# Kernel optimization log

Measured on AMD Instinct MI355X. Metric: run time of the kernel, lower is better.

The kernel has to match this reference:

```python
import jax, jax.numpy as jnp
import numpy as np

EPS = 1e-5
GROUPS = 8

def group_norm(x, w, b):
    B, C, H, W = x.shape
    xg = x.reshape(B, GROUPS, C // GROUPS, H, W)
    mean = xg.mean(axis=(2, 3, 4), keepdims=True)
    var = xg.var(axis=(2, 3, 4), keepdims=True)
    xn = ((xg - mean) * jax.lax.rsqrt(var + EPS)).reshape(B, C, H, W)
    return xn * w[None, :, None, None] + b[None, :, None, None]

def conv1x1(x, w, b):
    # x: [B,C,H,W], w: [O,C] -> [B,O,H,W]
    return jnp.einsum('bchw,oc->bohw', x, w) + b[None, :, None, None]

def setup_inputs() -> dict:
    key = jax.random.key(0)
    ks = jax.random.split(key, 16)
    C, Ci = 256, 128
    B, H, W = 4, 64, 64
    s3 = 1.0 / np.sqrt(C * 9)
    s1 = 1.0 / np.sqrt(C)
    return {
        'x': jax.random.normal(ks[0], (B, C, H, W), jnp.float32),
        'smooth_w': jax.random.uniform(ks[1], (C, C, 3, 3), jnp.float32, -s3, s3),
        'smooth_b': jax.random.uniform(ks[2], (C,), jnp.float32, -s3, s3),
        'gn1_w': jnp.ones((C,), jnp.float32),
        'gn1_b': jnp.zeros((C,), jnp.float32),
        'g_w': jax.random.uniform(ks[3], (Ci, C), jnp.float32, -s1, s1),
        'g_b': jax.random.uniform(ks[4], (Ci,), jnp.float32, -s1, s1),
        'theta_w': jax.random.uniform(ks[5], (Ci, C), jnp.float32, -s1, s1),
        'theta_b': jax.random.uniform(ks[6], (Ci,), jnp.float32, -s1, s1),
        'phi_w': jax.random.uniform(ks[7], (Ci, C), jnp.float32, -s1, s1),
        'phi_b': jax.random.uniform(ks[8], (Ci,), jnp.float32, -s1, s1),
        'w_w': 0.01 * jax.random.normal(ks[9], (C, Ci), jnp.float32),
        'w_b': jnp.zeros((C,), jnp.float32),
        'gn2_w': jnp.ones((C,), jnp.float32),
        'gn2_b': jnp.zeros((C,), jnp.float32),
    }

def reference(x, smooth_w, smooth_b, gn1_w, gn1_b, g_w, g_b, theta_w, theta_b,
              phi_w, phi_b, w_w, w_b, gn2_w, gn2_b):
    # input_smooth: 3x3 conv + GroupNorm(8) + ReLU
    xs = jax.lax.conv_general_dilated(
        x, smooth_w, window_strides=(1, 1), padding='SAME',
        dimension_numbers=('NCHW', 'OIHW', 'NCHW')) + smooth_b[None, :, None, None]
    xs = jax.nn.relu(group_norm(xs, gn1_w, gn1_b))
    B, C, H, W = xs.shape
    Ci = g_w.shape[0]
    N = H * W
    g_x = conv1x1(xs, g_w, g_b).reshape(B, Ci, N).transpose(0, 2, 1)      # [B,N,Ci]
    theta_x = conv1x1(xs, theta_w, theta_b).reshape(B, Ci, N).transpose(0, 2, 1)  # [B,N,Ci]
    phi_x = conv1x1(xs, phi_w, phi_b).reshape(B, Ci, N)                   # [B,Ci,N]
    f = jnp.einsum('bnc,bcm->bnm', theta_x, phi_x)                        # [B,N,N]
    attn = jax.nn.softmax(f, axis=-1)
    y = jnp.einsum('bnm,bmc->bnc', attn, g_x)                             # [B,N,Ci]
    y = y.transpose(0, 2, 1).reshape(B, Ci, H, W)
    w_y = group_norm(conv1x1(y, w_w, w_b), gn2_w, gn2_b)
    return w_y * 0.1 + xs
```

## Files before the change

### kernel.cpp

```cpp
#include <hip/hip_runtime.h>
#include <math.h>

#define Bn 4
#define Cn 256
#define CIn 128
#define Hn 64
#define Wn 64
#define Nn 4096
#define Gn 8
#define CPGn 32
#define EPSc 1e-5f

typedef unsigned short ushort_t;
typedef short bfrag __attribute__((ext_vector_type(8)));
typedef float f32x4 __attribute__((ext_vector_type(4)));
typedef ushort_t u16x8 __attribute__((ext_vector_type(8)));

static __device__ __forceinline__ ushort_t f2bf(float f) {
  unsigned u = __float_as_uint(f);
  return (ushort_t)((u + 0x7FFFu + ((u >> 16) & 1u)) >> 16);
}

static __device__ __forceinline__ unsigned cvt_pk_bf16(float lo, float hi) {
  unsigned r;
  asm("v_cvt_pk_bf16_f32 %0, %1, %2" : "=v"(r) : "v"(lo), "v"(hi));
  return r;
}

static __device__ __forceinline__ float bf2f(ushort_t u) {
  return __uint_as_float((unsigned)u << 16);
}

static __device__ __forceinline__ void gl_lds16(const ushort_t* g, ushort_t* l) {
  __builtin_amdgcn_global_load_lds(
      (__attribute__((address_space(1))) void*)g,
      (__attribute__((address_space(3))) void*)l, 16, 0, 0);
}

__global__ __launch_bounds__(256) void k_prepack(
    const float* __restrict__ w3, const float* __restrict__ thw,
    const float* __restrict__ phw, const float* __restrict__ gww,
    const float* __restrict__ ww,
    ushort_t* __restrict__ w9, ushort_t* __restrict__ wp9,
    ushort_t* __restrict__ wwb) {
  int i = blockIdx.x * 256 + threadIdx.x;
  if (i < 589824) {
    float v = w3[i];
    int co = i / 2304, r = i % 2304, ci = r / 9, tap = r % 9;
    w9[tap * 65536 + co * 256 + ci] = f2bf(v);
  } else if (i < 688128) {
    int j = i - 589824;
    int which = j >> 15, r = j & 32767;
    const float* src = (which == 0) ? thw : (which == 1) ? phw : gww;
    wp9[j] = f2bf(src[r]);
  } else if (i < 720896) {
    int j = i - 688128;
    wwb[j] = f2bf(ww[j]);
  }
}

__global__ __launch_bounds__(512) void k_conv_mfma(
    const float* __restrict__ x, const ushort_t* __restrict__ w9,
    const float* __restrict__ b3, float* __restrict__ out,
    float* __restrict__ part) {
  __shared__ __align__(16) ushort_t lx[3 * 66 * 128];
  const int tid = threadIdx.x;
  const int lane = tid & 63, w = tid >> 6;
  const int ln = lane & 15, lhi = lane >> 4;
  const int h = blockIdx.x, b = blockIdx.y;
  const int wco = w * 32;

  f32x4 acc[2][4];
#pragma unroll
  for (int mf = 0; mf < 2; ++mf)
#pragma unroll
    for (int nf = 0; nf < 4; ++nf) acc[mf][nf] = (f32x4){0.f, 0.f, 0.f, 0.f};

  for (int cc = 0; cc < 2; ++cc) {
    __syncthreads();
    for (int i = tid; i < 768; i += 512) {
      int dh = i / 256, r = i % 256, wpz = (r >> 7) ? 65 : 0, ci = r & 127;
      int off = (((dh * 66 + wpz) * 128 + ci) * 2) ^ ((wpz & 7) << 4);
      *(ushort_t*)((char*)lx + off) = 0;
    }
    for (int i = tid; i < 6144; i += 512) {
      int dh = i >> 11, r = i & 2047, ci = r >> 4, w4 = (r & 15) * 4;
      int hh = h + dh - 1;
      float4 v = {0.f, 0.f, 0.f, 0.f};
      if (hh >= 0 && hh < Hn)
        v = *(const float4*)(x + (((size_t)(b * Cn + cc * 128 + ci)) * Hn + hh) * Wn + w4);
      float vv[4] = {v.x, v.y, v.z, v.w};
#pragma unroll
      for (int j = 0; j < 4; ++j) {
        int wp = 1 + w4 + j;
        int off = (((dh * 66 + wp) * 128 + ci) * 2) ^ ((wp & 7) << 4);
        *(ushort_t*)((char*)lx + off) = f2bf(vv[j]);
      }
    }
    __syncthreads();

#pragma unroll
    for (int tap = 0; tap < 9; ++tap) {
      const int dh = tap / 3, dw = tap % 3;
#pragma unroll
      for (int kb = 0; kb < 4; ++kb) {
        const ushort_t* ap = w9 + tap * 65536 + (size_t)(wco + ln) * 256 +
                             cc * 128 + kb * 32 + lhi * 8;
        bfrag af0 = *(const bfrag*)ap;
        bfrag af1 = *(const bfrag*)(ap + 16 * 256);
        __builtin_amdgcn_s_setprio(1);
#pragma unroll
        for (int nf = 0; nf < 4; ++nf) {
          int wp = nf * 16 + ln + dw;
          int off = (((dh * 66 + wp) * 128 + kb * 32 + lhi * 8) * 2) ^ ((wp & 7) << 4);
          bfrag bf = *(const bfrag*)((const char*)lx + off);
          acc[0][nf] = __builtin_amdgcn_mfma_f32_16x16x32_bf16(af0, bf, acc[0][nf], 0, 0, 0);
          acc[1][nf] = __builtin_amdgcn_mfma_f32_16x16x32_bf16(af1, bf, acc[1][nf], 0, 0, 0);
        }
        __builtin_amdgcn_s_setprio(0);
      }
    }
  }

  float s_ = 0.f, q_ = 0.f;
#pragma unroll
  for (int mf = 0; mf < 2; ++mf) {
    float4 bv = *(const float4*)(b3 + wco + mf * 16 + lhi * 4);
    float bb[4] = {bv.x, bv.y, bv.z, bv.w};
#pragma unroll
    for (int nf = 0; nf < 4; ++nf) {
#pragma unroll
      for (int r = 0; r < 4; ++r) {
        int co = wco + mf * 16 + lhi * 4 + r;
        float v = acc[mf][nf][r] + bb[r];
        out[((size_t)(b * Cn + co)) * Nn + h * Wn + nf * 16 + ln] = v;
        s_ += v;
        q_ += v * v;
      }
    }
  }
#pragma unroll
  for (int off = 32; off; off >>= 1) {
    s_ += __shfl_xor(s_, off);
    q_ += __shfl_xor(q_, off);
  }
  if (lane == 0) {
    size_t pi = ((size_t)(b * Gn + w) * 64 + h) * 2;
    part[pi] = s_;
    part[pi + 1] = q_;
  }
}

__global__ void k_gn_final(const float* __restrict__ part, float* __restrict__ stats) {
  const int t = threadIdx.x;
  if (t < Bn * Gn) {
    float s = 0.f, ss = 0.f;
    for (int j = 0; j < 64; ++j) {
      s += part[(t * 64 + j) * 2];
      ss += part[(t * 64 + j) * 2 + 1];
    }
    const float inv = 1.f / (float)(CPGn * Nn);
    float mean = s * inv;
    float var = ss * inv - mean * mean;
    stats[t * 2] = mean;
    stats[t * 2 + 1] = rsqrtf(var + EPSc);
  }
}

__global__ __launch_bounds__(256) void k_gn1_apply_t(
    const float* __restrict__ xr, const float* __restrict__ stats,
    const float* __restrict__ gw, const float* __restrict__ gb,
    float* __restrict__ xs, ushort_t* __restrict__ xsT) {
  __shared__ ushort_t lt[32 * 64];
  const int t = threadIdx.x;
  const int n0 = blockIdx.x * 64, c0 = blockIdx.y * 32, b = blockIdx.z;
#pragma unroll
  for (int p = 0; p < 8; ++p) {
    int c = c0 + p * 4 + (t >> 6);
    int n = n0 + (t & 63);
    int bg = b * Gn + (c >> 5);
    float mean = stats[bg * 2], rstd = stats[bg * 2 + 1];
    float sc = gw[c] * rstd;
    float sb = gb[c] - mean * sc;
    size_t idx = ((size_t)(b * Cn + c)) * Nn + n;
    float val = fmaxf(xr[idx] * sc + sb, 0.f);
    xs[idx] = val;
    lt[(c - c0) * 64 + (t & 63)] = f2bf(val);
  }
  __syncthreads();
  {
    int n = t >> 2, cg = t & 3;
    u16x8 pk;
#pragma unroll
    for (int j = 0; j < 8; ++j) pk[j] = lt[(cg * 8 + j) * 64 + n];
    *(u16x8*)(xsT + ((size_t)(b * Nn + n0 + n)) * Cn + c0 + cg * 8) = pk;
  }
}

__global__ __launch_bounds__(256) void k_proj_mfma(
    const ushort_t* __restrict__ xsT, const ushort_t* __restrict__ wp9,
    const float* __restrict__ thb, const float* __restrict__ phb,
    const float* __restrict__ gbb,
    ushort_t* __restrict__ theta_b, ushort_t* __restrict__ phi_b,
    ushort_t* __restrict__ g_b) {
  __shared__ __align__(16) ushort_t lxs[64 * 256];
  const int tid = threadIdx.x;
  const int lane = tid & 63, w = tid >> 6;
  const int ln = lane & 15, lhi = lane >> 4;
  const int n0 = blockIdx.x * 64, which = blockIdx.y, b = blockIdx.z;
  const int wci = w * 32;

  for (int i = tid; i < 2048; i += 256) {
    int n = i >> 5, cchunk = (i & 31) * 8;
    uint4 v = *(const uint4*)(xsT + ((size_t)(b * Nn + n0 + n)) * Cn + cchunk);
    int off = ((n * 256 + cchunk) * 2) ^ ((n & 7) << 4);
    *(uint4*)((char*)lxs + off) = v;
  }
  __syncthreads();

  f32x4 acc[2][4];
#pragma unroll
  for (int mf = 0; mf < 2; ++mf)
#pragma unroll
    for (int nf = 0; nf < 4; ++nf) acc[mf][nf] = (f32x4){0.f, 0.f, 0.f, 0.f};

#pragma unroll
  for (int kb = 0; kb < 8; ++kb) {
    const ushort_t* ap = wp9 + which * 32768 + (size_t)(wci + ln) * 256 + kb * 32 + lhi * 8;
    bfrag af0 = *(const bfrag*)ap;
    bfrag af1 = *(const bfrag*)(ap + 16 * 256);
    __builtin_amdgcn_s_setprio(1);
#pragma unroll
    for (int nf = 0; nf < 4; ++nf) {
      int n = nf * 16 + ln;
      int off = ((n * 256 + kb * 32 + lhi * 8) * 2) ^ ((n & 7) << 4);
      bfrag bf = *(const bfrag*)((const char*)lxs + off);
      acc[0][nf] = __builtin_amdgcn_mfma_f32_16x16x32_bf16(af0, bf, acc[0][nf], 0, 0, 0);
      acc[1][nf] = __builtin_amdgcn_mfma_f32_16x16x32_bf16(af1, bf, acc[1][nf], 0, 0, 0);
    }
    __builtin_amdgcn_s_setprio(0);
  }

  const float* bs = (which == 0) ? thb : (which == 1) ? phb : gbb;
#pragma unroll
  for (int mf = 0; mf < 2; ++mf) {
    float4 bv = *(const float4*)(bs + wci + mf * 16 + lhi * 4);
    float bb[4] = {bv.x, bv.y, bv.z, bv.w};
    if (which < 2) {
      ushort_t* ob = ((which == 0) ? theta_b : phi_b) + (size_t)b * Nn * CIn;
#pragma unroll
      for (int nf = 0; nf < 4; ++nf) {
        int n = n0 + nf * 16 + ln;
        unsigned lo = (unsigned)f2bf(acc[mf][nf][0] + bb[0]) |
                      ((unsigned)f2bf(acc[mf][nf][1] + bb[1]) << 16);
        unsigned hi = (unsigned)f2bf(acc[mf][nf][2] + bb[2]) |
                      ((unsigned)f2bf(acc[mf][nf][3] + bb[3]) << 16);
        ushort_t* base = ob + (size_t)n * CIn + wci + mf * 16 + lhi * 4;
        *(unsigned*)base = lo;
        *(unsigned*)(base + 2) = hi;
      }
    } else {
      ushort_t* ob = g_b + (size_t)b * CIn * Nn;
#pragma unroll
      for (int nf = 0; nf < 4; ++nf) {
#pragma unroll
        for (int r = 0; r < 4; ++r) {
          int ci = wci + mf * 16 + lhi * 4 + r;
          ob[(size_t)ci * Nn + n0 + nf * 16 + ln] = f2bf(acc[mf][nf][r] + bb[r]);
        }
      }
    }
  }
}

__global__ __launch_bounds__(256) void k_attn_split(
    const ushort_t* __restrict__ theta_b, const ushort_t* __restrict__ phi_b,
    const ushort_t* __restrict__ g_b, ushort_t* __restrict__ ypart,
    float* __restrict__ mpart, float* __restrict__ lpart) {
  __shared__ __align__(16) ushort_t lphi[64 * 128];
  __shared__ __align__(16) ushort_t lg[128 * 64];
  __shared__ __align__(16) ushort_t lP[4][16 * 64];

  const int tid = threadIdx.x;
  const int lane = tid & 63, w = tid >> 6;
  const int ln = lane & 15, lhi = lane >> 4;

  const int bid = blockIdx.x;
  const int xcd = bid & 7, idx = bid >> 3;
  const int pair = xcd * 2 + (idx >> 6);
  const int b = pair >> 2, s = pair & 3;
  const int n0 = (idx & 63) * 64;
  const int kv0 = s * 1024;

  bfrag qf[4];
  {
    const ushort_t* thp =
        theta_b + ((size_t)(b * Nn + n0 + w * 16 + ln)) * CIn + 8 * lhi;
#pragma unroll
    for (int kb = 0; kb < 4; ++kb) qf[kb] = *(const bfrag*)(thp + kb * 32);
  }

  f32x4 yacc[8];
#pragma unroll
  for (int df = 0; df < 8; ++df) yacc[df] = (f32x4){0.f, 0.f, 0.f, 0.f};
  float mq = -3e38f, lq = 0.f;

  const ushort_t* gphi[4];
  const ushort_t* gg[4];
  ushort_t* ldphi[4];
  ushort_t* ldg[4];
#pragma unroll
  for (int k = 0; k < 4; ++k) {
    int ch = w * 4 + k;
    int boff = ch * 1024 + lane * 16;
    {
      int m = boff >> 8, c = (boff >> 4) & 15, cp = c ^ (m & 7);
      gphi[k] = phi_b + (size_t)b * Nn * CIn + (size_t)(kv0 + m) * CIn + cp * 8;
      ldphi[k] = lphi + ch * 512;
    }
    {
      int d = boff >> 7, c = (boff >> 4) & 7, cp = c ^ (d & 7);
      gg[k] = g_b + (size_t)b * CIn * Nn + (size_t)d * Nn + kv0 + cp * 8;
      ldg[k] = lg + ch * 512;
    }
  }
#pragma unroll
  for (int k = 0; k < 4; ++k) {
    gl_lds16(gphi[k], ldphi[k]);
    gl_lds16(gg[k], ldg[k]);
  }

  ushort_t* lPw = lP[w];

  for (int t = 0; t < 16; ++t) {
    __syncthreads();

    f32x4 sacc[4];
#pragma unroll
    for (int nf = 0; nf < 4; ++nf) sacc[nf] = (f32x4){0.f, 0.f, 0.f, 0.f};
    __builtin_amdgcn_s_setprio(1);
#pragma unroll
    for (int kb = 0; kb < 4; ++kb) {
#pragma unroll
      for (int nf = 0; nf < 4; ++nf) {
        int row = nf * 16 + ln;
        int off = ((row * 128 + kb * 32 + 8 * lhi) * 2) ^ ((ln & 7) << 4);
        bfrag pf = *(const bfrag*)((const char*)lphi + off);
        sacc[nf] = __builtin_amdgcn_mfma_f32_16x16x32_bf16(pf, qf[kb], sacc[nf], 0, 0, 0);
      }
    }
    __builtin_amdgcn_s_setprio(0);

    float mx;
    {
      float a0 = fmaxf(fmaxf(sacc[0][0], sacc[0][1]), fmaxf(sacc[0][2], sacc[0][3]));
      float a1 = fmaxf(fmaxf(sacc[1][0], sacc[1][1]), fmaxf(sacc[1][2], sacc[1][3]));
      float a2 = fmaxf(fmaxf(sacc[2][0], sacc[2][1]), fmaxf(sacc[2][2], sacc[2][3]));
      float a3 = fmaxf(fmaxf(sacc[3][0], sacc[3][1]), fmaxf(sacc[3][2], sacc[3][3]));
      mx = fmaxf(fmaxf(a0, a1), fmaxf(a2, a3));
    }
    mx = fmaxf(mx, __shfl_xor(mx, 16));
    mx = fmaxf(mx, __shfl_xor(mx, 32));
    float nm = fmaxf(mq, mx);
    float aaq = __expf(mq - nm);
    mq = nm;

    float psum = 0.f;
#pragma unroll
    for (int nf = 0; nf < 4; ++nf) {
      float p0 = __expf(sacc[nf][0] - nm);
      float p1 = __expf(sacc[nf][1] - nm);
      float p2 = __expf(sacc[nf][2] - nm);
      float p3 = __expf(sacc[nf][3] - nm);
      psum += (p0 + p1) + (p2 + p3);
      uint2 pk;
      pk.x = cvt_pk_bf16(p0, p1);
      pk.y = cvt_pk_bf16(p2, p3);
      int off = ((ln * 64 + nf * 16 + lhi * 4) * 2) ^ ((ln & 7) << 4);
      *(uint2*)((char*)lPw + off) = pk;
    }
    psum += __shfl_xor(psum, 16);
    psum += __shfl_xor(psum, 32);
    lq = lq * aaq + psum;

    float aar[4];
#pragma unroll
    for (int r = 0; r < 4; ++r) aar[r] = __shfl(aaq, 4 * lhi + r);
#pragma unroll
    for (int df = 0; df < 8; ++df)
#pragma unroll
      for (int r = 0; r < 4; ++r) yacc[df][r] *= aar[r];

    __builtin_amdgcn_s_setprio(1);
#pragma unroll
    for (int kb2 = 0; kb2 < 2; ++kb2) {
      int offa = ((ln * 64 + kb2 * 32 + 8 * lhi) * 2) ^ ((ln & 7) << 4);
      bfrag pa = *(const bfrag*)((const char*)lPw + offa);
#pragma unroll
      for (int df = 0; df < 8; ++df) {
        int d = df * 16 + ln;
        int offb = ((d * 64 + kb2 * 32 + 8 * lhi) * 2) ^ ((ln & 7) << 4);
        bfrag gbf = *(const bfrag*)((const char*)lg + offb);
        yacc[df] = __builtin_amdgcn_mfma_f32_16x16x32_bf16(pa, gbf, yacc[df], 0, 0, 0);
      }
    }
    __builtin_amdgcn_s_setprio(0);

    __syncthreads();
    if (t < 15) {
#pragma unroll
      for (int k = 0; k < 4; ++k) {
        gphi[k] += 64 * CIn;
        gg[k] += 64;
        gl_lds16(gphi[k], ldphi[k]);
        gl_lds16(gg[k], ldg[k]);
      }
    }
  }

  {
    ushort_t* ly = lphi;
#pragma unroll
    for (int df = 0; df < 8; ++df) {
#pragma unroll
      for (int r = 0; r < 4; ++r) {
        int q = w * 16 + lhi * 4 + r;
        int off = ((q * 128 + df * 16 + ln) * 2) ^ ((q & 7) << 4);
        *(ushort_t*)((char*)ly + off) = f2bf(yacc[df][r]);
      }
    }
  }
  __syncthreads();
  {
    int q = tid >> 2, c0 = (tid & 3) * 32;
    ushort_t* yp = ypart + ((size_t)((b * 4 + s) * Nn + n0 + q)) * CIn + c0;
#pragma unroll
    for (int k = 0; k < 4; ++k) {
      int off = ((q * 128 + c0 + k * 8) * 2) ^ ((q & 7) << 4);
      uint4 v = *(const uint4*)((const char*)lphi + off);
      *(uint4*)(yp + k * 8) = v;
    }
  }
  if (lhi == 0) {
    size_t qi = (size_t)(b * 4 + s) * Nn + n0 + w * 16 + ln;
    mpart[qi] = mq;
    lpart[qi] = lq;
  }
}

__global__ __launch_bounds__(512) void k_wconv_mfma(
    const ushort_t* __restrict__ ypart, const float* __restrict__ mpart,
    const float* __restrict__ lpart, const ushort_t* __restrict__ wwb,
    const float* __restrict__ wb, float* __restrict__ wy,
    float* __restrict__ part) {
  __shared__ __align__(16) ushort_t lyt[64 * 128];
  __shared__ float fSc[4][64];
  const int tid = threadIdx.x;
  const int lane = tid & 63, w = tid >> 6;
  const int ln = lane & 15, lhi = lane >> 4;
  const int n0 = blockIdx.x * 64, b = blockIdx.y;
  const int wco = w * 32;

  if (tid < 64) {
    int n = n0 + tid;
    float m0 = mpart[(size_t)(b * 4 + 0) * Nn + n], l0 = lpart[(size_t)(b * 4 + 0) * Nn + n];
    float m1 = mpart[(size_t)(b * 4 + 1) * Nn + n], l1 = lpart[(size_t)(b * 4 + 1) * Nn + n];
    float m2 = mpart[(size_t)(b * 4 + 2) * Nn + n], l2 = lpart[(size_t)(b * 4 + 2) * Nn + n];
    float m3 = mpart[(size_t)(b * 4 + 3) * Nn + n], l3 = lpart[(size_t)(b * 4 + 3) * Nn + n];
    float M = fmaxf(fmaxf(m0, m1), fmaxf(m2, m3));
    float s0 = __expf(m0 - M), s1 = __expf(m1 - M), s2 = __expf(m2 - M), s3 = __expf(m3 - M);
    float inv = 1.f / (s0 * l0 + s1 * l1 + s2 * l2 + s3 * l3);
    fSc[0][tid] = s0 * inv;
    fSc[1][tid] = s1 * inv;
    fSc[2][tid] = s2 * inv;
    fSc[3][tid] = s3 * inv;
  }
  __syncthreads();

  for (int i = tid; i < 1024; i += 512) {
    int n = i >> 4, ch = (i & 15) * 8;
    float f0 = fSc[0][n], f1 = fSc[1][n], f2 = fSc[2][n], f3 = fSc[3][n];
    const ushort_t* yb = ypart + ((size_t)(b * 4) * Nn + n0 + n) * CIn + ch;
    const size_t sstr = (size_t)Nn * CIn;
    u16x8 v0 = *(const u16x8*)(yb);
    u16x8 v1 = *(const u16x8*)(yb + sstr);
    u16x8 v2 = *(const u16x8*)(yb + 2 * sstr);
    u16x8 v3 = *(const u16x8*)(yb + 3 * sstr);
    float a[8];
#pragma unroll
    for (int j = 0; j < 8; ++j)
      a[j] = f0 * bf2f(v0[j]) + f1 * bf2f(v1[j]) + f2 * bf2f(v2[j]) + f3 * bf2f(v3[j]);
    uint4 pk;
    pk.x = cvt_pk_bf16(a[0], a[1]);
    pk.y = cvt_pk_bf16(a[2], a[3]);
    pk.z = cvt_pk_bf16(a[4], a[5]);
    pk.w = cvt_pk_bf16(a[6], a[7]);
    int off = ((n * 128 + ch) * 2) ^ ((n & 7) << 4);
    *(uint4*)((char*)lyt + off) = pk;
  }
  __syncthreads();

  f32x4 acc[2][4];
#pragma unroll
  for (int mf = 0; mf < 2; ++mf)
#pragma unroll
    for (int nf = 0; nf < 4; ++nf) acc[mf][nf] = (f32x4){0.f, 0.f, 0.f, 0.f};

#pragma unroll
  for (int kb = 0; kb < 4; ++kb) {
    const ushort_t* ap = wwb + (size_t)(wco + ln) * CIn + kb * 32 + lhi * 8;
    bfrag af0 = *(const bfrag*)ap;
    bfrag af1 = *(const bfrag*)(ap + 16 * CIn);
    __builtin_amdgcn_s_setprio(1);
#pragma unroll
    for (int nf = 0; nf < 4; ++nf) {
      int n = nf * 16 + ln;
      int off = ((n * 128 + kb * 32 + lhi * 8) * 2) ^ ((n & 7) << 4);
      bfrag bf = *(const bfrag*)((const char*)lyt + off);
      acc[0][nf] = __builtin_amdgcn_mfma_f32_16x16x32_bf16(af0, bf, acc[0][nf], 0, 0, 0);
      acc[1][nf] = __builtin_amdgcn_mfma_f32_16x16x32_bf16(af1, bf, acc[1][nf], 0, 0, 0);
    }
    __builtin_amdgcn_s_setprio(0);
  }

  float s_ = 0.f, q_ = 0.f;
#pragma unroll
  for (int mf = 0; mf < 2; ++mf) {
    float4 bv = *(const float4*)(wb + wco + mf * 16 + lhi * 4);
    float bb[4] = {bv.x, bv.y, bv.z, bv.w};
#pragma unroll
    for (int nf = 0; nf < 4; ++nf) {
#pragma unroll
      for (int r = 0; r < 4; ++r) {
        int co = wco + mf * 16 + lhi * 4 + r;
        float v = acc[mf][nf][r] + bb[r];
        wy[((size_t)(b * Cn + co)) * Nn + n0 + nf * 16 + ln] = v;
        s_ += v;
        q_ += v * v;
      }
    }
  }
#pragma unroll
  for (int off = 32; off; off >>= 1) {
    s_ += __shfl_xor(s_, off);
    q_ += __shfl_xor(q_, off);
  }
  if (lane == 0) {
    size_t pi = ((size_t)(b * Gn + w) * 64 + blockIdx.x) * 2;
    part[pi] = s_;
    part[pi + 1] = q_;
  }
}

__global__ __launch_bounds__(256) void k_final(
    const float* __restrict__ wy, const float* __restrict__ stats,
    const float* __restrict__ g2w, const float* __restrict__ g2b,
    const float* __restrict__ xs, float* __restrict__ out) {
  size_t i = ((size_t)blockIdx.x * 256 + threadIdx.x) * 4;
  int c = (int)((i >> 12) & 255);
  int bg = (int)(i >> 20) * Gn + (c >> 5);
  float mean = stats[bg * 2], rstd = stats[bg * 2 + 1];
  float sc = g2w[c] * rstd * 0.1f;
  float sb = (g2b[c] - mean * rstd * g2w[c]) * 0.1f;
  float4 v = *(const float4*)(wy + i);
  float4 xv = *(const float4*)(xs + i);
  v.x = v.x * sc + sb + xv.x;
  v.y = v.y * sc + sb + xv.y;
  v.z = v.z * sc + sb + xv.z;
  v.w = v.w * sc + sb + xv.w;
  *(float4*)(out + i) = v;
}

extern "C" void kernel_launch(void* const* d_in, const int* in_sizes, int n_in,
                              void* d_out, int out_size, void* d_ws, size_t ws_size,
                              hipStream_t stream) {
  (void)in_sizes; (void)n_in; (void)out_size; (void)ws_size;
  const float* x   = (const float*)d_in[0];
  const float* sw  = (const float*)d_in[1];
  const float* sb  = (const float*)d_in[2];
  const float* g1w = (const float*)d_in[3];
  const float* g1b = (const float*)d_in[4];
  const float* gw  = (const float*)d_in[5];
  const float* gb  = (const float*)d_in[6];
  const float* thw = (const float*)d_in[7];
  const float* thb = (const float*)d_in[8];
  const float* phw = (const float*)d_in[9];
  const float* phb = (const float*)d_in[10];
  const float* ww  = (const float*)d_in[11];
  const float* wb  = (const float*)d_in[12];
  const float* g2w = (const float*)d_in[13];
  const float* g2b = (const float*)d_in[14];
  float* out = (float*)d_out;
  float* ws = (float*)d_ws;

  float*    xs_raw  = ws;
  float*    xs      = ws + 4194304;
  ushort_t* theta_b = (ushort_t*)(ws + 10486912);
  ushort_t* phi_b   = (ushort_t*)(ws + 11535488);
  ushort_t* g_b     = (ushort_t*)(ws + 12584064);
  ushort_t* xsT     = (ushort_t*)(ws + 13632640);
  ushort_t* w9      = (ushort_t*)(ws + 15729792);
  ushort_t* wp9     = (ushort_t*)(ws + 16024704);
  ushort_t* wwb     = (ushort_t*)(ws + 16073856);
  float*    wy      = ws + 10486912;
  ushort_t* ypart   = (ushort_t*)xs_raw;
  float*    mpart   = ws + 16090240;
  float*    lpart   = ws + 16155776;
  float*    part    = ws + 16221312;
  float*    st1     = ws + 16225408;
  float*    st2     = ws + 16225472;

  k_prepack<<<2816, 256, 0, stream>>>(sw, thw, phw, gw, ww, w9, wp9, wwb);
  k_conv_mfma<<<dim3(Hn, Bn), 512, 0, stream>>>(x, w9, sb, xs_raw, part);
  k_gn_final<<<1, 64, 0, stream>>>(part, st1);
  k_gn1_apply_t<<<dim3(64, 8, 4), 256, 0, stream>>>(xs_raw, st1, g1w, g1b, xs, xsT);
  k_proj_mfma<<<dim3(64, 3, 4), 256, 0, stream>>>(xsT, wp9, thb, phb, gb,
                                                  theta_b, phi_b, g_b);
  k_attn_split<<<1024, 256, 0, stream>>>(theta_b, phi_b, g_b, ypart, mpart, lpart);
  k_wconv_mfma<<<dim3(64, 4), 512, 0, stream>>>(ypart, mpart, lpart, wwb, wb, wy, part);
  k_gn_final<<<1, 64, 0, stream>>>(part, st2);
  k_final<<<4096, 256, 0, stream>>>(wy, st2, g2w, g2b, xs, out);
}
```

Before: 168.1 us.

## Store conv and GN intermediates in bf16 and pre-transpose input for async LDS loads

Adds a pre-pass that transposes x into channel-last bf16, so the 3x3 conv can fill shared memory with direct global-to-LDS 16-byte loads instead of per-element strided fp32 loads with conversion. The raw conv output, the GN1 output xs, and the wconv output wy are now written and read as bf16 instead of fp32, roughly halving traffic in the apply and final kernels. This costs an extra kernel launch and transpose pass, and adds precision loss in the residual path and GN2 input.

New measurement: 161.5 us (median of 2 runs). -3.9%, faster.

```diff
diff --git a/kernel.cpp b/kernel.cpp
--- a/kernel.cpp
+++ b/kernel.cpp
@@ -59,9 +59,30 @@
   }
 }
 
+__global__ __launch_bounds__(256) void k_xT(
+    const float* __restrict__ x, ushort_t* __restrict__ xbT) {
+  __shared__ ushort_t lt[32 * 64];
+  const int t = threadIdx.x;
+  const int n0 = blockIdx.x * 64, c0 = blockIdx.y * 32, b = blockIdx.z;
+#pragma unroll
+  for (int p = 0; p < 8; ++p) {
+    int c = c0 + p * 4 + (t >> 6);
+    int n = n0 + (t & 63);
+    lt[(c - c0) * 64 + (t & 63)] = f2bf(x[((size_t)(b * Cn + c)) * Nn + n]);
+  }
+  __syncthreads();
+  {
+    int n = t >> 2, cg = t & 3;
+    u16x8 pk;
+#pragma unroll
+    for (int j = 0; j < 8; ++j) pk[j] = lt[(cg * 8 + j) * 64 + n];
+    *(u16x8*)(xbT + ((size_t)(b * Nn + n0 + n)) * Cn + c0 + cg * 8) = pk;
+  }
+}
+
 __global__ __launch_bounds__(512) void k_conv_mfma(
-    const float* __restrict__ x, const ushort_t* __restrict__ w9,
-    const float* __restrict__ b3, float* __restrict__ out,
+    const ushort_t* __restrict__ xbT, const ushort_t* __restrict__ w9,
+    const float* __restrict__ b3, ushort_t* __restrict__ xr_b,
     float* __restrict__ part) {
   __shared__ __align__(16) ushort_t lx[3 * 66 * 128];
   const int tid = threadIdx.x;
@@ -70,6 +91,12 @@
   const int h = blockIdx.x, b = blockIdx.y;
   const int wco = w * 32;
 
+  for (int i = tid; i < 768; i += 512) {
+    int dh = i / 256, r = i % 256, wpz = (r >> 7) ? 65 : 0, ci = r & 127;
+    int off = (((dh * 66 + wpz) * 128 + ci) * 2) ^ ((wpz & 7) << 4);
+    *(ushort_t*)((char*)lx + off) = 0;
+  }
+
   f32x4 acc[2][4];
 #pragma unroll
   for (int mf = 0; mf < 2; ++mf)
@@ -78,23 +105,20 @@
 
   for (int cc = 0; cc < 2; ++cc) {
     __syncthreads();
-    for (int i = tid; i < 768; i += 512) {
-      int dh = i / 256, r = i % 256, wpz = (r >> 7) ? 65 : 0, ci = r & 127;
-      int off = (((dh * 66 + wpz) * 128 + ci) * 2) ^ ((wpz & 7) << 4);
-      *(ushort_t*)((char*)lx + off) = 0;
-    }
-    for (int i = tid; i < 6144; i += 512) {
-      int dh = i >> 11, r = i & 2047, ci = r >> 4, w4 = (r & 15) * 4;
+#pragma unroll
+    for (int k = 0; k < 6; ++k) {
+      int ch = w * 6 + k;
+      int dh = ch >> 4, wq = (ch & 15) * 4;
+      int rowl = wq + (lane >> 4);
+      int wp = rowl + 1;
       int hh = h + dh - 1;
-      float4 v = {0.f, 0.f, 0.f, 0.f};
-      if (hh >= 0 && hh < Hn)
-        v = *(const float4*)(x + (((size_t)(b * Cn + cc * 128 + ci)) * Hn + hh) * Wn + w4);
-      float vv[4] = {v.x, v.y, v.z, v.w};
-#pragma unroll
-      for (int j = 0; j < 4; ++j) {
-        int wp = 1 + w4 + j;
-        int off = (((dh * 66 + wp) * 128 + ci) * 2) ^ ((wp & 7) << 4);
-        *(ushort_t*)((char*)lx + off) = f2bf(vv[j]);
+      ushort_t* dst = lx + (dh * 66 + wq + 1) * 128;
+      if (hh >= 0 && hh < Hn) {
+        int srcC = (((lane & 15) ^ (wp & 7)) * 8) + cc * 128;
+        gl_lds16(xbT + ((size_t)(b * Nn + hh * Wn + rowl)) * Cn + srcC, dst);
+      } else {
+        *(uint4*)((char*)lx + (((dh * 66 + wq + 1) * 128 + lane * 8) * 2)) =
+            (uint4){0u, 0u, 0u, 0u};
       }
     }
     __syncthreads();
@@ -133,7 +157,7 @@
       for (int r = 0; r < 4; ++r) {
         int co = wco + mf * 16 + lhi * 4 + r;
         float v = acc[mf][nf][r] + bb[r];
-        out[((size_t)(b * Cn + co)) * Nn + h * Wn + nf * 16 + ln] = v;
+        xr_b[((size_t)(b * Cn + co)) * Nn + h * Wn + nf * 16 + ln] = f2bf(v);
         s_ += v;
         q_ += v * v;
       }
@@ -168,24 +192,28 @@
 }
 
 __global__ __launch_bounds__(256) void k_gn1_apply_t(
-    const float* __restrict__ xr, const float* __restrict__ stats,
+    const ushort_t* __restrict__ xr_b, const float* __restrict__ stats,
     const float* __restrict__ gw, const float* __restrict__ gb,
-    float* __restrict__ xs, ushort_t* __restrict__ xsT) {
+    ushort_t* __restrict__ xs_b, ushort_t* __restrict__ xsT) {
   __shared__ ushort_t lt[32 * 64];
   const int t = threadIdx.x;
   const int n0 = blockIdx.x * 64, c0 = blockIdx.y * 32, b = blockIdx.z;
-#pragma unroll
-  for (int p = 0; p < 8; ++p) {
-    int c = c0 + p * 4 + (t >> 6);
-    int n = n0 + (t & 63);
+  {
+    int c = c0 + (t >> 3);
+    int nc = (t & 7) * 8;
     int bg = b * Gn + (c >> 5);
     float mean = stats[bg * 2], rstd = stats[bg * 2 + 1];
     float sc = gw[c] * rstd;
     float sb = gb[c] - mean * sc;
-    size_t idx = ((size_t)(b * Cn + c)) * Nn + n;
-    float val = fmaxf(xr[idx] * sc + sb, 0.f);
-    xs[idx] = val;
-    lt[(c - c0) * 64 + (t & 63)] = f2bf(val);
+    size_t idx = ((size_t)(b * Cn + c)) * Nn + n0 + nc;
+    u16x8 v = *(const u16x8*)(xr_b + idx);
+    u16x8 o;
+#pragma unroll
+    for (int j = 0; j < 8; ++j)
+      o[j] = f2bf(fmaxf(bf2f(v[j]) * sc + sb, 0.f));
+    *(u16x8*)(xs_b + idx) = o;
+#pragma unroll
+    for (int j = 0; j < 8; ++j) lt[(c - c0) * 64 + nc + j] = o[j];
   }
   __syncthreads();
   {
@@ -451,7 +479,7 @@
 __global__ __launch_bounds__(512) void k_wconv_mfma(
     const ushort_t* __restrict__ ypart, const float* __restrict__ mpart,
     const float* __restrict__ lpart, const ushort_t* __restrict__ wwb,
-    const float* __restrict__ wb, float* __restrict__ wy,
+    const float* __restrict__ wb, ushort_t* __restrict__ wy_b,
     float* __restrict__ part) {
   __shared__ __align__(16) ushort_t lyt[64 * 128];
   __shared__ float fSc[4][64];
@@ -534,7 +562,7 @@
       for (int r = 0; r < 4; ++r) {
         int co = wco + mf * 16 + lhi * 4 + r;
         float v = acc[mf][nf][r] + bb[r];
-        wy[((size_t)(b * Cn + co)) * Nn + n0 + nf * 16 + ln] = v;
+        wy_b[((size_t)(b * Cn + co)) * Nn + n0 + nf * 16 + ln] = f2bf(v);
         s_ += v;
         q_ += v * v;
       }
@@ -553,22 +581,28 @@
 }
 
 __global__ __launch_bounds__(256) void k_final(
-    const float* __restrict__ wy, const float* __restrict__ stats,
+    const ushort_t* __restrict__ wy_b, const float* __restrict__ stats,
     const float* __restrict__ g2w, const float* __restrict__ g2b,
-    const float* __restrict__ xs, float* __restrict__ out) {
-  size_t i = ((size_t)blockIdx.x * 256 + threadIdx.x) * 4;
+    const ushort_t* __restrict__ xs_b, float* __restrict__ out) {
+  size_t i = ((size_t)blockIdx.x * 256 + threadIdx.x) * 8;
   int c = (int)((i >> 12) & 255);
   int bg = (int)(i >> 20) * Gn + (c >> 5);
   float mean = stats[bg * 2], rstd = stats[bg * 2 + 1];
   float sc = g2w[c] * rstd * 0.1f;
   float sb = (g2b[c] - mean * rstd * g2w[c]) * 0.1f;
-  float4 v = *(const float4*)(wy + i);
-  float4 xv = *(const float4*)(xs + i);
-  v.x = v.x * sc + sb + xv.x;
-  v.y = v.y * sc + sb + xv.y;
-  v.z = v.z * sc + sb + xv.z;
-  v.w = v.w * sc + sb + xv.w;
-  *(float4*)(out + i) = v;
+  u16x8 wv = *(const u16x8*)(wy_b + i);
+  u16x8 xv = *(const u16x8*)(xs_b + i);
+  float4 o0, o1;
+  o0.x = bf2f(wv[0]) * sc + sb + bf2f(xv[0]);
+  o0.y = bf2f(wv[1]) * sc + sb + bf2f(xv[1]);
+  o0.z = bf2f(wv[2]) * sc + sb + bf2f(xv[2]);
+  o0.w = bf2f(wv[3]) * sc + sb + bf2f(xv[3]);
+  o1.x = bf2f(wv[4]) * sc + sb + bf2f(xv[4]);
+  o1.y = bf2f(wv[5]) * sc + sb + bf2f(xv[5]);
+  o1.z = bf2f(wv[6]) * sc + sb + bf2f(xv[6]);
+  o1.w = bf2f(wv[7]) * sc + sb + bf2f(xv[7]);
+  *(float4*)(out + i) = o0;
+  *(float4*)(out + i + 4) = o1;
 }
 
 extern "C" void kernel_launch(void* const* d_in, const int* in_sizes, int n_in,
@@ -593,8 +627,10 @@
   float* out = (float*)d_out;
   float* ws = (float*)d_ws;
 
-  float*    xs_raw  = ws;
-  float*    xs      = ws + 4194304;
+  ushort_t* xr_b    = (ushort_t*)ws;
+  ushort_t* ypart   = (ushort_t*)ws;
+  ushort_t* xs_b    = (ushort_t*)(ws + 4194304);
+  ushort_t* xbT     = (ushort_t*)(ws + 6291456);
   ushort_t* theta_b = (ushort_t*)(ws + 10486912);
   ushort_t* phi_b   = (ushort_t*)(ws + 11535488);
   ushort_t* g_b     = (ushort_t*)(ws + 12584064);
@@ -602,8 +638,7 @@
   ushort_t* w9      = (ushort_t*)(ws + 15729792);
   ushort_t* wp9     = (ushort_t*)(ws + 16024704);
   ushort_t* wwb     = (ushort_t*)(ws + 16073856);
-  float*    wy      = ws + 10486912;
-  ushort_t* ypart   = (ushort_t*)xs_raw;
+  ushort_t* wy_b    = (ushort_t*)(ws + 10486912);
   float*    mpart   = ws + 16090240;
   float*    lpart   = ws + 16155776;
   float*    part    = ws + 16221312;
@@ -611,13 +646,14 @@
   float*    st2     = ws + 16225472;
 
   k_prepack<<<2816, 256, 0, stream>>>(sw, thw, phw, gw, ww, w9, wp9, wwb);
-  k_conv_mfma<<<dim3(Hn, Bn), 512, 0, stream>>>(x, w9, sb, xs_raw, part);
+  k_xT<<<dim3(64, 8, 4), 256, 0, stream>>>(x, xbT);
+  k_conv_mfma<<<dim3(Hn, Bn), 512, 0, stream>>>(xbT, w9, sb, xr_b, part);
   k_gn_final<<<1, 64, 0, stream>>>(part, st1);
-  k_gn1_apply_t<<<dim3(64, 8, 4), 256, 0, stream>>>(xs_raw, st1, g1w, g1b, xs, xsT);
+  k_gn1_apply_t<<<dim3(64, 8, 4), 256, 0, stream>>>(xr_b, st1, g1w, g1b, xs_b, xsT);
   k_proj_mfma<<<dim3(64, 3, 4), 256, 0, stream>>>(xsT, wp9, thb, phb, gb,
                                                   theta_b, phi_b, g_b);
   k_attn_split<<<1024, 256, 0, stream>>>(theta_b, phi_b, g_b, ypart, mpart, lpart);
-  k_wconv_mfma<<<dim3(64, 4), 512, 0, stream>>>(ypart, mpart, lpart, wwb, wb, wy, part);
+  k_wconv_mfma<<<dim3(64, 4), 512, 0, stream>>>(ypart, mpart, lpart, wwb, wb, wy_b, part);
   k_gn_final<<<1, 64, 0, stream>>>(part, st2);
-  k_final<<<4096, 256, 0, stream>>>(wy, st2, g2w, g2b, xs, out);
-}
+  k_final<<<2048, 256, 0, stream>>>(wy_b, st2, g2w, g2b, xs_b, out);
+}
```
